# Kernel optimization log

Measured on AMD Instinct MI355X. Metric: run time of the kernel, lower is better.

## Reference

```python
import jax, jax.numpy as jnp
import numpy as np

B, S, H = 16, 512, 768
NH, DH = 12, 64  # heads, head dim (H = NH*DH)
E = 8            # number of experts


def setup_inputs() -> dict:
    key = jax.random.key(0)
    ks = jax.random.split(key, 9)
    w_scale = 1.0 / np.sqrt(H).astype(np.float32)
    return {
        "hidden_states": jax.random.normal(ks[0], (B, S, H), jnp.float32),
        "attention_mask": jnp.zeros((B, 1, 1, S), jnp.float32),
        "Wq": jax.random.normal(ks[1], (E, H, H), jnp.float32) * w_scale,
        "bq": jnp.zeros((E, H), jnp.float32),
        "Wk": jax.random.normal(ks[2], (E, H, H), jnp.float32) * w_scale,
        "bk": jnp.zeros((E, H), jnp.float32),
        "Wv": jax.random.normal(ks[3], (E, H, H), jnp.float32) * w_scale,
        "bv": jnp.zeros((E, H), jnp.float32),
        "expert_idx": jax.random.randint(ks[4], (B,), 0, E, jnp.int64),
    }


def reference(hidden_states, attention_mask, Wq, bq, Wk, bk, Wv, bv, expert_idx):
    b, s, h = hidden_states.shape

    def proj(W, bias):
        # Per-sample expert selection: math-equivalent to computing all experts
        # then slice_for_expert, but gathers weights instead of activations.
        Wg = W[expert_idx]            # [B, H_out, H_in]
        bg = bias[expert_idx]         # [B, H_out]
        y = jnp.einsum('bsd,bod->bso', hidden_states, Wg) + bg[:, None, :]
        return y.reshape(b, s, NH, DH).transpose(0, 2, 1, 3)  # [B, NH, S, DH]

    q = proj(Wq, bq)
    k = proj(Wk, bk)
    v = proj(Wv, bv)

    scores = jnp.einsum('bhqd,bhkd->bhqk', q, k) / np.sqrt(DH).astype(np.float32)
    scores = scores + attention_mask
    probs = jax.nn.softmax(scores, axis=-1)  # dropout p=0.0 (eval)
    ctx = jnp.einsum('bhqk,bhkd->bhqd', probs, v)
    return ctx.transpose(0, 2, 1, 3).reshape(b, s, h)
```

## Files before the change

kernel.cpp:

```cpp
#include <hip/hip_runtime.h>
#include <hip/hip_bf16.h>
#include <stdint.h>

typedef __bf16 bf16;
typedef bf16 bf16x8 __attribute__((ext_vector_type(8)));
typedef bf16 bf16x4 __attribute__((ext_vector_type(4)));
typedef float f32x4 __attribute__((ext_vector_type(4)));

#define MFMA_16x16x32(a, b, c) __builtin_amdgcn_mfma_f32_16x16x32_bf16((a), (b), (c), 0, 0, 0)

constexpr int B = 16, S = 512, H = 768, NH = 12, DH = 64;
constexpr long NHID = (long)B * S * H;
constexpr long NW = (long)8 * H * H;

constexpr size_t XB_OFF = 0;
constexpr size_t XB_SZ  = (size_t)NHID * 2;
constexpr size_t W_SZ   = (size_t)NW * 2;
constexpr size_t WQ_OFF = XB_OFF + XB_SZ;
constexpr size_t WK_OFF = WQ_OFF + W_SZ;
constexpr size_t WV_OFF = WK_OFF + W_SZ;
constexpr size_t PROJ_SZ = (size_t)B * NH * S * DH * 2;
constexpr size_t QB_OFF = WV_OFF + W_SZ;
constexpr size_t KB_OFF = QB_OFF + PROJ_SZ;
constexpr size_t VB_OFF = KB_OFF + PROJ_SZ;
constexpr size_t WS_NEED = VB_OFF + PROJ_SZ;

__global__ void cvt_all(const float* __restrict__ x,
                        const float* __restrict__ wq, const float* __restrict__ wk,
                        const float* __restrict__ wv,
                        bf16* __restrict__ xb, bf16* __restrict__ wqb,
                        bf16* __restrict__ wkb, bf16* __restrict__ wvb) {
  long i = ((long)blockIdx.x * blockDim.x + threadIdx.x) * 8;
  const float* src;
  bf16* dst;
  long off;
  if (i < NHID)               { src = x;  dst = xb;  off = i; }
  else if (i < NHID + NW)     { src = wq; dst = wqb; off = i - NHID; }
  else if (i < NHID + 2 * NW) { src = wk; dst = wkb; off = i - NHID - NW; }
  else if (i < NHID + 3 * NW) { src = wv; dst = wvb; off = i - NHID - 2 * NW; }
  else return;
  const float4* sp = reinterpret_cast<const float4*>(src + off);
  float4 a = sp[0], b = sp[1];
  bf16x8 o;
  o[0] = (bf16)a.x; o[1] = (bf16)a.y; o[2] = (bf16)a.z; o[3] = (bf16)a.w;
  o[4] = (bf16)b.x; o[5] = (bf16)b.y; o[6] = (bf16)b.z; o[7] = (bf16)b.w;
  *reinterpret_cast<bf16x8*>(dst + off) = o;
}

__global__ __launch_bounds__(512, 2) void proj_gemm(
    const bf16* __restrict__ Xb,
    const bf16* __restrict__ Wqb, const bf16* __restrict__ Wkb, const bf16* __restrict__ Wvb,
    const float* __restrict__ bq, const float* __restrict__ bk, const float* __restrict__ bv,
    const int* __restrict__ eidx,
    bf16* __restrict__ Qb, bf16* __restrict__ Kb, bf16* __restrict__ Vb)
{
  __shared__ __align__(16) bf16 As[2][256 * 32];
  __shared__ __align__(16) bf16 Bs[2][128 * 32];

  const int xcd = blockIdx.x & 7;
  const int bi  = blockIdx.x >> 3;
  const int b   = xcd * 2 + (bi / 36);
  const int rem = bi % 36;
  const int m0  = (rem / 18) * 256;
  const int gy  = rem % 18;
  const int proj = gy / 6;
  const int n0 = (gy % 6) * 128;
  const int e = eidx[b];

  const bf16* W = (proj == 0 ? Wqb : (proj == 1 ? Wkb : Wvb)) + (size_t)e * H * H;
  const float* bias = (proj == 0 ? bq : (proj == 1 ? bk : bv)) + (size_t)e * H;
  bf16* Out = (proj == 0 ? Qb : (proj == 1 ? Kb : Vb));

  const int tid = threadIdx.x;
  const int lane = tid & 63;
  const int wave = tid >> 6;
  const int wm = wave >> 1, wn = wave & 1;
  const int r = lane & 15, lg = lane >> 4;

  const bf16* Abase = Xb + ((size_t)b * S + m0) * H;
  const bf16* Bbase = W + (size_t)n0 * H;

  const int srow = lane >> 2;
  const int sg = ((lane & 3) ^ ((lane >> 3) & 3)) * 8;

  auto stage = [&](int kt, int pb) {
    const int k0 = kt * 32;
#pragma unroll
    for (int i = 0; i < 2; ++i) {
      const int seg = wave * 2 + i;
      const bf16* ga = Abase + (size_t)(seg * 16 + srow) * H + k0 + sg;
      __builtin_amdgcn_global_load_lds(
          (const __attribute__((address_space(1))) void*)ga,
          (__attribute__((address_space(3))) void*)(&As[pb][seg * 512]), 16, 0, 0);
    }
    const bf16* gb = Bbase + (size_t)(wave * 16 + srow) * H + k0 + sg;
    __builtin_amdgcn_global_load_lds(
        (const __attribute__((address_space(1))) void*)gb,
        (__attribute__((address_space(3))) void*)(&Bs[pb][wave * 512]), 16, 0, 0);
  };

  f32x4 acc[4][4] = {};

  stage(0, 0);
  __syncthreads();

  const int sz = (r >> 1) & 3;

  int buf = 0;
#pragma unroll 1
  for (int kt = 0; kt < 24; ++kt) {
    if (kt < 23) stage(kt + 1, buf ^ 1);

    bf16x8 af[4], bfr[4];
#pragma unroll
    for (int mi = 0; mi < 4; ++mi)
      af[mi] = *reinterpret_cast<const bf16x8*>(
          &As[buf][(wm * 64 + mi * 16 + r) * 32 + ((lg ^ sz) * 8)]);
#pragma unroll
    for (int ni = 0; ni < 4; ++ni)
      bfr[ni] = *reinterpret_cast<const bf16x8*>(
          &Bs[buf][(wn * 64 + ni * 16 + r) * 32 + ((lg ^ sz) * 8)]);
#pragma unroll
    for (int mi = 0; mi < 4; ++mi)
#pragma unroll
      for (int ni = 0; ni < 4; ++ni)
        acc[mi][ni] = MFMA_16x16x32(af[mi], bfr[ni], acc[mi][ni]);

    __syncthreads();
    buf ^= 1;
  }

  if (proj != 2) {
#pragma unroll
    for (int ni = 0; ni < 4; ++ni) {
      const int col = n0 + wn * 64 + ni * 16 + r;
      const int nh = col >> 6, dh = col & 63;
      const float bb = bias[col];
      bf16* orow = Out + ((size_t)b * NH + nh) * S * DH + dh;
#pragma unroll
      for (int mi = 0; mi < 4; ++mi) {
#pragma unroll
        for (int rr = 0; rr < 4; ++rr) {
          const int srow2 = m0 + wm * 64 + mi * 16 + lg * 4 + rr;
          orow[(size_t)srow2 * DH] = (bf16)(acc[mi][ni][rr] + bb);
        }
      }
    }
  } else {
#pragma unroll
    for (int ni = 0; ni < 4; ++ni) {
      const int col = n0 + wn * 64 + ni * 16 + r;
      const int nh = col >> 6, dh = col & 63;
      const float bb = bias[col];
      bf16* orow = Out + ((size_t)b * NH + nh) * DH * S + (size_t)dh * S;
#pragma unroll
      for (int mi = 0; mi < 4; ++mi) {
        bf16x4 v;
#pragma unroll
        for (int rr = 0; rr < 4; ++rr) v[rr] = (bf16)(acc[mi][ni][rr] + bb);
        *reinterpret_cast<bf16x4*>(orow + m0 + wm * 64 + mi * 16 + lg * 4) = v;
      }
    }
  }
}

__global__ __launch_bounds__(256, 4) void attn_kernel(
    const bf16* __restrict__ Qb, const bf16* __restrict__ Kb, const bf16* __restrict__ VTb,
    const float* __restrict__ mask, float* __restrict__ out)
{
  __shared__ __align__(16) bf16 Ks[2][64 * 64];
  __shared__ __align__(16) bf16 Vs[2][64 * 64];
  __shared__ float maskS[512];

  const int x = blockIdx.x;
  const int xcd = x & 7;
  const int grp = x >> 3;
  const int qblk = grp & 7;
  const int bh = (grp >> 3) * 8 + xcd;
  const int b = bh / NH;
  const int h = bh % NH;
  const int tid = threadIdx.x;
  const int wave = tid >> 6;
  const int lane = tid & 63;
  const int r = lane & 15, lg = lane >> 4;
  const int q0 = qblk * 64 + wave * 16;

  const bf16* Q  = Qb  + (size_t)bh * S * DH;
  const bf16* K  = Kb  + (size_t)bh * S * DH;
  const bf16* VT = VTb + (size_t)bh * DH * S;

  for (int i = tid; i < S; i += 256) maskS[i] = mask[b * S + i];

  const int srowoff = lane >> 3;
  const int sg = (lane & 7) ^ srowoff;

  auto stage = [&](int kt, int buf) {
    const int kb = kt * 64;
#pragma unroll
    for (int i = 0; i < 2; ++i) {
      const int c = wave * 2 + i;
      const int row = c * 8 + srowoff;
      const bf16* gk = K + (size_t)(kb + row) * DH + sg * 8;
      __builtin_amdgcn_global_load_lds(
          (const __attribute__((address_space(1))) void*)gk,
          (__attribute__((address_space(3))) void*)(&Ks[buf][c * 512]), 16, 0, 0);
      const bf16* gv = VT + (size_t)row * S + kb + sg * 8;
      __builtin_amdgcn_global_load_lds(
          (const __attribute__((address_space(1))) void*)gv,
          (__attribute__((address_space(3))) void*)(&Vs[buf][c * 512]), 16, 0, 0);
    }
  };

  const bf16x8 qf0 = *reinterpret_cast<const bf16x8*>(&Q[(size_t)(q0 + r) * DH + lg * 8]);
  const bf16x8 qf1 = *reinterpret_cast<const bf16x8*>(&Q[(size_t)(q0 + r) * DH + 32 + lg * 8]);

  stage(0, 0);
  __syncthreads();

  float m = -3.0e38f, l = 0.0f;
  f32x4 ctx[4] = {};
  int buf = 0;

#pragma unroll 1
  for (int kt = 0; kt < 8; ++kt) {
    const int kb = kt * 64;
    if (kt < 7) stage(kt + 1, buf ^ 1);

    f32x4 sa[4];
#pragma unroll
    for (int t = 0; t < 4; ++t) {
      const int row = t * 16 + r;
      const int sw = row & 7;
      bf16x8 kf0 = *reinterpret_cast<const bf16x8*>(&Ks[buf][row * 64 + ((lg ^ sw) * 8)]);
      bf16x8 kf1 = *reinterpret_cast<const bf16x8*>(&Ks[buf][row * 64 + (((lg + 4) ^ sw) * 8)]);
      f32x4 a = {};
      a = MFMA_16x16x32(kf0, qf0, a);
      a = MFMA_16x16x32(kf1, qf1, a);
      sa[t] = a;
    }

    float tmax = -3.0e38f;
#pragma unroll
    for (int t = 0; t < 4; ++t)
#pragma unroll
      for (int rr = 0; rr < 4; ++rr) {
        float s = sa[t][rr] * 0.125f + maskS[kb + t * 16 + lg * 4 + rr];
        sa[t][rr] = s;
        tmax = fmaxf(tmax, s);
      }
    tmax = fmaxf(tmax, __shfl_xor(tmax, 16));
    tmax = fmaxf(tmax, __shfl_xor(tmax, 32));
    const float mnew = fmaxf(m, tmax);
    const float scale = __expf(m - mnew);
    m = mnew;
    float ps = 0.f;
#pragma unroll
    for (int t = 0; t < 4; ++t)
#pragma unroll
      for (int rr = 0; rr < 4; ++rr) {
        float p = __expf(sa[t][rr] - mnew);
        sa[t][rr] = p;
        ps += p;
      }
    l = l * scale + ps;
#pragma unroll
    for (int dt = 0; dt < 4; ++dt) ctx[dt] *= scale;

#pragma unroll
    for (int kc = 0; kc < 2; ++kc) {
      bf16x8 pf;
      f32x4 p0 = sa[2 * kc], p1 = sa[2 * kc + 1];
      pf[0] = (bf16)p0[0]; pf[1] = (bf16)p0[1]; pf[2] = (bf16)p0[2]; pf[3] = (bf16)p0[3];
      pf[4] = (bf16)p1[0]; pf[5] = (bf16)p1[1]; pf[6] = (bf16)p1[2]; pf[7] = (bf16)p1[3];
      const int chunk_lo = kc * 4 + (lg >> 1);
      const int rem = (lg & 1) * 4;
#pragma unroll
      for (int dt = 0; dt < 4; ++dt) {
        const int row = dt * 16 + r;
        const int sw = row & 7;
        const bf16* vlo = &Vs[buf][row * 64 + ((chunk_lo ^ sw) * 8) + rem];
        const bf16* vhi = &Vs[buf][row * 64 + (((chunk_lo + 2) ^ sw) * 8) + rem];
        bf16x4 lo = *reinterpret_cast<const bf16x4*>(vlo);
        bf16x4 hi = *reinterpret_cast<const bf16x4*>(vhi);
        bf16x8 vf;
        vf[0] = lo[0]; vf[1] = lo[1]; vf[2] = lo[2]; vf[3] = lo[3];
        vf[4] = hi[0]; vf[5] = hi[1]; vf[6] = hi[2]; vf[7] = hi[3];
        ctx[dt] = MFMA_16x16x32(vf, pf, ctx[dt]);
      }
    }

    __syncthreads();
    buf ^= 1;
  }

  l += __shfl_xor(l, 16);
  l += __shfl_xor(l, 32);
  const float inv = 1.0f / l;

  float* obase = out + ((size_t)b * S + q0 + r) * H + h * DH;
#pragma unroll
  for (int dt = 0; dt < 4; ++dt) {
    float4 o;
    o.x = ctx[dt][0] * inv; o.y = ctx[dt][1] * inv;
    o.z = ctx[dt][2] * inv; o.w = ctx[dt][3] * inv;
    *reinterpret_cast<float4*>(obase + dt * 16 + lg * 4) = o;
  }
}

extern "C" void kernel_launch(void* const* d_in, const int* in_sizes, int n_in,
                              void* d_out, int out_size, void* d_ws, size_t ws_size,
                              hipStream_t stream) {
  const float* hidden = (const float*)d_in[0];
  const float* mask   = (const float*)d_in[1];
  const float* Wq = (const float*)d_in[2];
  const float* bq = (const float*)d_in[3];
  const float* Wk = (const float*)d_in[4];
  const float* bk = (const float*)d_in[5];
  const float* Wv = (const float*)d_in[6];
  const float* bv = (const float*)d_in[7];
  const int* eidx = (const int*)d_in[8];

  if (ws_size < WS_NEED) return;

  char* ws = (char*)d_ws;
  bf16* Xb  = (bf16*)(ws + XB_OFF);
  bf16* Wqb = (bf16*)(ws + WQ_OFF);
  bf16* Wkb = (bf16*)(ws + WK_OFF);
  bf16* Wvb = (bf16*)(ws + WV_OFF);
  bf16* Qbf = (bf16*)(ws + QB_OFF);
  bf16* Kbf = (bf16*)(ws + KB_OFF);
  bf16* Vbf = (bf16*)(ws + VB_OFF);
  float* out = (float*)d_out;

  cvt_all<<<9984, 256, 0, stream>>>(hidden, Wq, Wk, Wv, Xb, Wqb, Wkb, Wvb);
  proj_gemm<<<576, 512, 0, stream>>>(Xb, Wqb, Wkb, Wvb, bq, bk, bv, eidx,
                                     Qbf, Kbf, Vbf);
  attn_kernel<<<1536, 256, 0, stream>>>(Qbf, Kbf, Vbf, mask, out);
}
```

Baseline: 102.9 us.

## Load V fragments from global into registers and skip rescale when max stable

V tiles are no longer staged through LDS. Each wave now loads its V fragments straight from global memory into registers at the start of each key tile. This halves LDS use and raises the occupancy hint from 4 to 6 blocks per CU. The online softmax also skips the running-max rescale of ctx and l when the new tile max stays within 6 of the current max, a lazy-rescale trick. The costs are extra global traffic per wave, since V is no longer shared across waves, higher register pressure from holding the V fragments, and a bounded exp overflow risk from the threshold.

Result: slower. 180.8 us (+75.7%).

```diff
diff --git a/kernel.cpp b/kernel.cpp
--- a/kernel.cpp
+++ b/kernel.cpp
@@ -164,12 +164,11 @@
   }
 }
 
-__global__ __launch_bounds__(256, 4) void attn_kernel(
+__global__ __launch_bounds__(256, 6) void attn_kernel(
     const bf16* __restrict__ Qb, const bf16* __restrict__ Kb, const bf16* __restrict__ VTb,
     const float* __restrict__ mask, float* __restrict__ out)
 {
   __shared__ __align__(16) bf16 Ks[2][64 * 64];
-  __shared__ __align__(16) bf16 Vs[2][64 * 64];
   __shared__ float maskS[512];
 
   const int x = blockIdx.x;
@@ -204,10 +203,6 @@
       __builtin_amdgcn_global_load_lds(
           (const __attribute__((address_space(1))) void*)gk,
           (__attribute__((address_space(3))) void*)(&Ks[buf][c * 512]), 16, 0, 0);
-      const bf16* gv = VT + (size_t)row * S + kb + sg * 8;
-      __builtin_amdgcn_global_load_lds(
-          (const __attribute__((address_space(1))) void*)gv,
-          (__attribute__((address_space(3))) void*)(&Vs[buf][c * 512]), 16, 0, 0);
     }
   };
 
@@ -225,6 +220,16 @@
   for (int kt = 0; kt < 8; ++kt) {
     const int kb = kt * 64;
     if (kt < 7) stage(kt + 1, buf ^ 1);
+
+    bf16x4 vlo[4][2], vhi[4][2];
+#pragma unroll
+    for (int dt = 0; dt < 4; ++dt)
+#pragma unroll
+      for (int kc = 0; kc < 2; ++kc) {
+        const bf16* vr = &VT[(size_t)(dt * 16 + r) * S + kb + kc * 32 + lg * 4];
+        vlo[dt][kc] = *reinterpret_cast<const bf16x4*>(vr);
+        vhi[dt][kc] = *reinterpret_cast<const bf16x4*>(vr + 16);
+      }
 
     f32x4 sa[4];
 #pragma unroll
@@ -250,21 +255,24 @@
       }
     tmax = fmaxf(tmax, __shfl_xor(tmax, 16));
     tmax = fmaxf(tmax, __shfl_xor(tmax, 32));
-    const float mnew = fmaxf(m, tmax);
-    const float scale = __expf(m - mnew);
-    m = mnew;
+    if (!__all(tmax <= m + 6.0f)) {
+      const float mnew = fmaxf(m, tmax);
+      const float scale = __expf(m - mnew);
+      l *= scale;
+#pragma unroll
+      for (int dt = 0; dt < 4; ++dt) ctx[dt] *= scale;
+      m = mnew;
+    }
     float ps = 0.f;
 #pragma unroll
     for (int t = 0; t < 4; ++t)
 #pragma unroll
       for (int rr = 0; rr < 4; ++rr) {
-        float p = __expf(sa[t][rr] - mnew);
+        float p = __expf(sa[t][rr] - m);
         sa[t][rr] = p;
         ps += p;
       }
-    l = l * scale + ps;
-#pragma unroll
-    for (int dt = 0; dt < 4; ++dt) ctx[dt] *= scale;
+    l += ps;
 
 #pragma unroll
     for (int kc = 0; kc < 2; ++kc) {
@@ -272,17 +280,10 @@
       f32x4 p0 = sa[2 * kc], p1 = sa[2 * kc + 1];
       pf[0] = (bf16)p0[0]; pf[1] = (bf16)p0[1]; pf[2] = (bf16)p0[2]; pf[3] = (bf16)p0[3];
       pf[4] = (bf16)p1[0]; pf[5] = (bf16)p1[1]; pf[6] = (bf16)p1[2]; pf[7] = (bf16)p1[3];
-      const int chunk_lo = kc * 4 + (lg >> 1);
-      const int rem = (lg & 1) * 4;
 #pragma unroll
       for (int dt = 0; dt < 4; ++dt) {
-        const int row = dt * 16 + r;
-        const int sw = row & 7;
-        const bf16* vlo = &Vs[buf][row * 64 + ((chunk_lo ^ sw) * 8) + rem];
-        const bf16* vhi = &Vs[buf][row * 64 + (((chunk_lo + 2) ^ sw) * 8) + rem];
-        bf16x4 lo = *reinterpret_cast<const bf16x4*>(vlo);
-        bf16x4 hi = *reinterpret_cast<const bf16x4*>(vhi);
         bf16x8 vf;
+        bf16x4 lo = vlo[dt][kc], hi = vhi[dt][kc];
         vf[0] = lo[0]; vf[1] = lo[1]; vf[2] = lo[2]; vf[3] = lo[3];
         vf[4] = hi[0]; vf[5] = hi[1]; vf[6] = hi[2]; vf[7] = hi[3];
         ctx[dt] = MFMA_16x16x32(vf, pf, ctx[dt]);
```

## Triple-buffer projection GEMM with split MFMA phases and priority hints

Applied to the files above, without the earlier changes.

The projection GEMM moves from double-buffered to triple-buffered LDS staging, prefetching two k-tiles ahead. Waits on outstanding global loads now use an explicit vmcnt count instead of a full __syncthreads. Each k-step's MFMAs are split into two halves separated by a barrier, with s_setprio raised around the MFMA bursts to interleave waves. The goal is to hide global-to-LDS latency and improve MFMA issue overlap. In exchange it uses more LDS, which may reduce occupancy, and the hand-set vmcnt values depend on the exact number of loads issued per stage.

Result: slower. 106.1 us (+3.1%).

```diff
diff --git a/kernel.cpp b/kernel.cpp
--- a/kernel.cpp
+++ b/kernel.cpp
@@ -54,8 +54,8 @@
     const int* __restrict__ eidx,
     bf16* __restrict__ Qb, bf16* __restrict__ Kb, bf16* __restrict__ Vb)
 {
-  __shared__ __align__(16) bf16 As[2][256 * 32];
-  __shared__ __align__(16) bf16 Bs[2][128 * 32];
+  __shared__ __align__(16) bf16 As[3][256 * 32];
+  __shared__ __align__(16) bf16 Bs[3][128 * 32];
 
   const int xcd = blockIdx.x & 7;
   const int bi  = blockIdx.x >> 3;
@@ -102,32 +102,58 @@
   f32x4 acc[4][4] = {};
 
   stage(0, 0);
-  __syncthreads();
+  stage(1, 1);
+  asm volatile("s_waitcnt vmcnt(3)" ::: "memory");
+  __builtin_amdgcn_s_barrier();
 
   const int sz = (r >> 1) & 3;
 
   int buf = 0;
 #pragma unroll 1
   for (int kt = 0; kt < 24; ++kt) {
-    if (kt < 23) stage(kt + 1, buf ^ 1);
-
-    bf16x8 af[4], bfr[4];
+    const int nb = (buf >= 1) ? buf - 1 : 2;
+    if (kt + 2 < 24) stage(kt + 2, nb);
+
+    const bf16* Ab = &As[buf][0];
+    const bf16* Bb = &Bs[buf][0];
+
+    bf16x8 af[4], bflo[2];
 #pragma unroll
     for (int mi = 0; mi < 4; ++mi)
       af[mi] = *reinterpret_cast<const bf16x8*>(
-          &As[buf][(wm * 64 + mi * 16 + r) * 32 + ((lg ^ sz) * 8)]);
-#pragma unroll
-    for (int ni = 0; ni < 4; ++ni)
-      bfr[ni] = *reinterpret_cast<const bf16x8*>(
-          &Bs[buf][(wn * 64 + ni * 16 + r) * 32 + ((lg ^ sz) * 8)]);
-#pragma unroll
-    for (int mi = 0; mi < 4; ++mi)
-#pragma unroll
-      for (int ni = 0; ni < 4; ++ni)
-        acc[mi][ni] = MFMA_16x16x32(af[mi], bfr[ni], acc[mi][ni]);
-
-    __syncthreads();
-    buf ^= 1;
+          &Ab[(wm * 64 + mi * 16 + r) * 32 + ((lg ^ sz) * 8)]);
+#pragma unroll
+    for (int ni = 0; ni < 2; ++ni)
+      bflo[ni] = *reinterpret_cast<const bf16x8*>(
+          &Bb[(wn * 64 + ni * 16 + r) * 32 + ((lg ^ sz) * 8)]);
+    __builtin_amdgcn_s_setprio(1);
+#pragma unroll
+    for (int mi = 0; mi < 4; ++mi) {
+      acc[mi][0] = MFMA_16x16x32(af[mi], bflo[0], acc[mi][0]);
+      acc[mi][1] = MFMA_16x16x32(af[mi], bflo[1], acc[mi][1]);
+    }
+    __builtin_amdgcn_s_setprio(0);
+    __builtin_amdgcn_s_barrier();
+
+    bf16x8 bfhi[2];
+#pragma unroll
+    for (int ni = 0; ni < 2; ++ni)
+      bfhi[ni] = *reinterpret_cast<const bf16x8*>(
+          &Bb[(wn * 64 + (2 + ni) * 16 + r) * 32 + ((lg ^ sz) * 8)]);
+    __builtin_amdgcn_s_setprio(1);
+#pragma unroll
+    for (int mi = 0; mi < 4; ++mi) {
+      acc[mi][2] = MFMA_16x16x32(af[mi], bfhi[0], acc[mi][2]);
+      acc[mi][3] = MFMA_16x16x32(af[mi], bfhi[1], acc[mi][3]);
+    }
+    __builtin_amdgcn_s_setprio(0);
+
+    if (kt < 22)
+      asm volatile("s_waitcnt vmcnt(3)" ::: "memory");
+    else
+      asm volatile("s_waitcnt vmcnt(0)" ::: "memory");
+    __builtin_amdgcn_s_barrier();
+    buf = (buf == 2) ? 0 : buf + 1;
   }
 
   if (proj != 2) {
```

## Stage Q/K projection epilogue through LDS and double per-wave query rows in attention

Applied to the files above, without the earlier changes.

The Q/K projection epilogue previously wrote scattered scalar bf16 values with a 64-element stride. It now writes each wave's 64x64 tile into padded shared memory and then stores rows as coalesced 16-byte vectors. The attention kernel now has each wave process 32 query rows (two 16-row groups) instead of 16, so each K/V fragment loaded from LDS is reused across two MFMA groups. This halves the grid to 768 blocks and lowers the occupancy hint to 3, trading higher register pressure and less parallelism for fewer LDS reads and fewer K/V tile loads per query.

New measurement: 96.94 us. -5.8%, faster.

```diff
diff --git a/kernel.cpp b/kernel.cpp
--- a/kernel.cpp
+++ b/kernel.cpp
@@ -54,8 +54,9 @@
     const int* __restrict__ eidx,
     bf16* __restrict__ Qb, bf16* __restrict__ Kb, bf16* __restrict__ Vb)
 {
-  __shared__ __align__(16) bf16 As[2][256 * 32];
-  __shared__ __align__(16) bf16 Bs[2][128 * 32];
+  __shared__ __align__(16) char smem[73728];
+  bf16* Asb = (bf16*)smem;
+  bf16* Bsb = (bf16*)(smem + 32768);
 
   const int xcd = blockIdx.x & 7;
   const int bi  = blockIdx.x >> 3;
@@ -91,12 +92,12 @@
       const bf16* ga = Abase + (size_t)(seg * 16 + srow) * H + k0 + sg;
       __builtin_amdgcn_global_load_lds(
           (const __attribute__((address_space(1))) void*)ga,
-          (__attribute__((address_space(3))) void*)(&As[pb][seg * 512]), 16, 0, 0);
+          (__attribute__((address_space(3))) void*)(&Asb[pb * 8192 + seg * 512]), 16, 0, 0);
     }
     const bf16* gb = Bbase + (size_t)(wave * 16 + srow) * H + k0 + sg;
     __builtin_amdgcn_global_load_lds(
         (const __attribute__((address_space(1))) void*)gb,
-        (__attribute__((address_space(3))) void*)(&Bs[pb][wave * 512]), 16, 0, 0);
+        (__attribute__((address_space(3))) void*)(&Bsb[pb * 4096 + wave * 512]), 16, 0, 0);
   };
 
   f32x4 acc[4][4] = {};
@@ -115,11 +116,11 @@
 #pragma unroll
     for (int mi = 0; mi < 4; ++mi)
       af[mi] = *reinterpret_cast<const bf16x8*>(
-          &As[buf][(wm * 64 + mi * 16 + r) * 32 + ((lg ^ sz) * 8)]);
+          &Asb[buf * 8192 + (wm * 64 + mi * 16 + r) * 32 + ((lg ^ sz) * 8)]);
 #pragma unroll
     for (int ni = 0; ni < 4; ++ni)
       bfr[ni] = *reinterpret_cast<const bf16x8*>(
-          &Bs[buf][(wn * 64 + ni * 16 + r) * 32 + ((lg ^ sz) * 8)]);
+          &Bsb[buf * 4096 + (wn * 64 + ni * 16 + r) * 32 + ((lg ^ sz) * 8)]);
 #pragma unroll
     for (int mi = 0; mi < 4; ++mi)
 #pragma unroll
@@ -131,20 +132,25 @@
   }
 
   if (proj != 2) {
+    bf16* ep = (bf16*)smem + wave * 4352;
 #pragma unroll
     for (int ni = 0; ni < 4; ++ni) {
-      const int col = n0 + wn * 64 + ni * 16 + r;
-      const int nh = col >> 6, dh = col & 63;
-      const float bb = bias[col];
-      bf16* orow = Out + ((size_t)b * NH + nh) * S * DH + dh;
-#pragma unroll
-      for (int mi = 0; mi < 4; ++mi) {
-#pragma unroll
-        for (int rr = 0; rr < 4; ++rr) {
-          const int srow2 = m0 + wm * 64 + mi * 16 + lg * 4 + rr;
-          orow[(size_t)srow2 * DH] = (bf16)(acc[mi][ni][rr] + bb);
-        }
-      }
+      const int col = ni * 16 + r;
+      const float bb = bias[n0 + wn * 64 + col];
+#pragma unroll
+      for (int mi = 0; mi < 4; ++mi)
+#pragma unroll
+        for (int rr = 0; rr < 4; ++rr)
+          ep[(mi * 16 + lg * 4 + rr) * 68 + col] = (bf16)(acc[mi][ni][rr] + bb);
+    }
+    const int nh = (n0 + wn * 64) >> 6;
+    bf16* gb = Out + (((size_t)b * NH + nh) * S + (m0 + wm * 64)) * DH;
+    const int sub = lane & 7, rowL = lane >> 3;
+#pragma unroll
+    for (int pass = 0; pass < 8; ++pass) {
+      const int row = pass * 8 + rowL;
+      bf16x8 v = *reinterpret_cast<const bf16x8*>(&ep[row * 68 + sub * 8]);
+      *reinterpret_cast<bf16x8*>(&gb[(size_t)row * DH + sub * 8]) = v;
     }
   } else {
 #pragma unroll
@@ -164,7 +170,7 @@
   }
 }
 
-__global__ __launch_bounds__(256, 4) void attn_kernel(
+__global__ __launch_bounds__(256, 3) void attn_kernel(
     const bf16* __restrict__ Qb, const bf16* __restrict__ Kb, const bf16* __restrict__ VTb,
     const float* __restrict__ mask, float* __restrict__ out)
 {
@@ -175,15 +181,15 @@
   const int x = blockIdx.x;
   const int xcd = x & 7;
   const int grp = x >> 3;
-  const int qblk = grp & 7;
-  const int bh = (grp >> 3) * 8 + xcd;
+  const int qblk = grp & 3;
+  const int bh = (grp >> 2) * 8 + xcd;
   const int b = bh / NH;
   const int h = bh % NH;
   const int tid = threadIdx.x;
   const int wave = tid >> 6;
   const int lane = tid & 63;
   const int r = lane & 15, lg = lane >> 4;
-  const int q0 = qblk * 64 + wave * 16;
+  const int qbase = qblk * 128 + wave * 32;
 
   const bf16* Q  = Qb  + (size_t)bh * S * DH;
   const bf16* K  = Kb  + (size_t)bh * S * DH;
@@ -211,14 +217,20 @@
     }
   };
 
-  const bf16x8 qf0 = *reinterpret_cast<const bf16x8*>(&Q[(size_t)(q0 + r) * DH + lg * 8]);
-  const bf16x8 qf1 = *reinterpret_cast<const bf16x8*>(&Q[(size_t)(q0 + r) * DH + 32 + lg * 8]);
+  bf16x8 qf0[2], qf1[2];
+#pragma unroll
+  for (int g = 0; g < 2; ++g) {
+    const bf16* qr = &Q[(size_t)(qbase + g * 16 + r) * DH];
+    qf0[g] = *reinterpret_cast<const bf16x8*>(qr + lg * 8);
+    qf1[g] = *reinterpret_cast<const bf16x8*>(qr + 32 + lg * 8);
+  }
 
   stage(0, 0);
   __syncthreads();
 
-  float m = -3.0e38f, l = 0.0f;
-  f32x4 ctx[4] = {};
+  float mr[2] = {-3.0e38f, -3.0e38f};
+  float lr[2] = {0.f, 0.f};
+  f32x4 ctx[2][4] = {};
   int buf = 0;
 
 #pragma unroll 1
@@ -226,52 +238,63 @@
     const int kb = kt * 64;
     if (kt < 7) stage(kt + 1, buf ^ 1);
 
-    f32x4 sa[4];
+    f32x4 sa[2][4];
 #pragma unroll
     for (int t = 0; t < 4; ++t) {
       const int row = t * 16 + r;
       const int sw = row & 7;
       bf16x8 kf0 = *reinterpret_cast<const bf16x8*>(&Ks[buf][row * 64 + ((lg ^ sw) * 8)]);
       bf16x8 kf1 = *reinterpret_cast<const bf16x8*>(&Ks[buf][row * 64 + (((lg + 4) ^ sw) * 8)]);
-      f32x4 a = {};
-      a = MFMA_16x16x32(kf0, qf0, a);
-      a = MFMA_16x16x32(kf1, qf1, a);
-      sa[t] = a;
-    }
-
-    float tmax = -3.0e38f;
-#pragma unroll
-    for (int t = 0; t < 4; ++t)
-#pragma unroll
-      for (int rr = 0; rr < 4; ++rr) {
-        float s = sa[t][rr] * 0.125f + maskS[kb + t * 16 + lg * 4 + rr];
-        sa[t][rr] = s;
-        tmax = fmaxf(tmax, s);
+#pragma unroll
+      for (int g = 0; g < 2; ++g) {
+        f32x4 a = {};
+        a = MFMA_16x16x32(kf0, qf0[g], a);
+        a = MFMA_16x16x32(kf1, qf1[g], a);
+        sa[g][t] = a;
       }
-    tmax = fmaxf(tmax, __shfl_xor(tmax, 16));
-    tmax = fmaxf(tmax, __shfl_xor(tmax, 32));
-    const float mnew = fmaxf(m, tmax);
-    const float scale = __expf(m - mnew);
-    m = mnew;
-    float ps = 0.f;
-#pragma unroll
-    for (int t = 0; t < 4; ++t)
-#pragma unroll
-      for (int rr = 0; rr < 4; ++rr) {
-        float p = __expf(sa[t][rr] - mnew);
-        sa[t][rr] = p;
-        ps += p;
+    }
+
+#pragma unroll
+    for (int g = 0; g < 2; ++g) {
+      float tmax = -3.0e38f;
+#pragma unroll
+      for (int t = 0; t < 4; ++t)
+#pragma unroll
+        for (int rr = 0; rr < 4; ++rr) {
+          float s = sa[g][t][rr] * 0.125f + maskS[kb + t * 16 + lg * 4 + rr];
+          sa[g][t][rr] = s;
+          tmax = fmaxf(tmax, s);
+        }
+      tmax = fmaxf(tmax, __shfl_xor(tmax, 16));
+      tmax = fmaxf(tmax, __shfl_xor(tmax, 32));
+      const float mnew = fmaxf(mr[g], tmax);
+      const float scale = __expf(mr[g] - mnew);
+      mr[g] = mnew;
+      float ps = 0.f;
+#pragma unroll
+      for (int t = 0; t < 4; ++t)
+#pragma unroll
+        for (int rr = 0; rr < 4; ++rr) {
+          float p = __expf(sa[g][t][rr] - mnew);
+          sa[g][t][rr] = p;
+          ps += p;
+        }
+      lr[g] = lr[g] * scale + ps;
+#pragma unroll
+      for (int dt = 0; dt < 4; ++dt) ctx[g][dt] *= scale;
+    }
+
+#pragma unroll
+    for (int kc = 0; kc < 2; ++kc) {
+      bf16x8 pf[2];
+#pragma unroll
+      for (int g = 0; g < 2; ++g) {
+        f32x4 p0 = sa[g][2 * kc], p1 = sa[g][2 * kc + 1];
+        bf16x8 o;
+        o[0] = (bf16)p0[0]; o[1] = (bf16)p0[1]; o[2] = (bf16)p0[2]; o[3] = (bf16)p0[3];
+        o[4] = (bf16)p1[0]; o[5] = (bf16)p1[1]; o[6] = (bf16)p1[2]; o[7] = (bf16)p1[3];
+        pf[g] = o;
       }
-    l = l * scale + ps;
-#pragma unroll
-    for (int dt = 0; dt < 4; ++dt) ctx[dt] *= scale;
-
-#pragma unroll
-    for (int kc = 0; kc < 2; ++kc) {
-      bf16x8 pf;
-      f32x4 p0 = sa[2 * kc], p1 = sa[2 * kc + 1];
-      pf[0] = (bf16)p0[0]; pf[1] = (bf16)p0[1]; pf[2] = (bf16)p0[2]; pf[3] = (bf16)p0[3];
-      pf[4] = (bf16)p1[0]; pf[5] = (bf16)p1[1]; pf[6] = (bf16)p1[2]; pf[7] = (bf16)p1[3];
       const int chunk_lo = kc * 4 + (lg >> 1);
       const int rem = (lg & 1) * 4;
 #pragma unroll
@@ -285,7 +308,9 @@
         bf16x8 vf;
         vf[0] = lo[0]; vf[1] = lo[1]; vf[2] = lo[2]; vf[3] = lo[3];
         vf[4] = hi[0]; vf[5] = hi[1]; vf[6] = hi[2]; vf[7] = hi[3];
-        ctx[dt] = MFMA_16x16x32(vf, pf, ctx[dt]);
+#pragma unroll
+        for (int g = 0; g < 2; ++g)
+          ctx[g][dt] = MFMA_16x16x32(vf, pf[g], ctx[g][dt]);
       }
     }
 
@@ -293,17 +318,20 @@
     buf ^= 1;
   }
 
-  l += __shfl_xor(l, 16);
-  l += __shfl_xor(l, 32);
-  const float inv = 1.0f / l;
-
-  float* obase = out + ((size_t)b * S + q0 + r) * H + h * DH;
-#pragma unroll
-  for (int dt = 0; dt < 4; ++dt) {
-    float4 o;
-    o.x = ctx[dt][0] * inv; o.y = ctx[dt][1] * inv;
-    o.z = ctx[dt][2] * inv; o.w = ctx[dt][3] * inv;
-    *reinterpret_cast<float4*>(obase + dt * 16 + lg * 4) = o;
+#pragma unroll
+  for (int g = 0; g < 2; ++g) {
+    float l = lr[g];
+    l += __shfl_xor(l, 16);
+    l += __shfl_xor(l, 32);
+    const float inv = 1.0f / l;
+    float* obase = out + ((size_t)b * S + qbase + g * 16 + r) * H + h * DH;
+#pragma unroll
+    for (int dt = 0; dt < 4; ++dt) {
+      float4 o;
+      o.x = ctx[g][dt][0] * inv; o.y = ctx[g][dt][1] * inv;
+      o.z = ctx[g][dt][2] * inv; o.w = ctx[g][dt][3] * inv;
+      *reinterpret_cast<float4*>(obase + dt * 16 + lg * 4) = o;
+    }
   }
 }
 
@@ -335,5 +363,5 @@
   cvt_all<<<9984, 256, 0, stream>>>(hidden, Wq, Wk, Wv, Xb, Wqb, Wkb, Wvb);
   proj_gemm<<<576, 512, 0, stream>>>(Xb, Wqb, Wkb, Wvb, bq, bk, bv, eidx,
                                      Qbf, Kbf, Vbf);
-  attn_kernel<<<1536, 256, 0, stream>>>(Qbf, Kbf, Vbf, mask, out);
+  attn_kernel<<<768, 256, 0, stream>>>(Qbf, Kbf, Vbf, mask, out);
 }
```
